# Kernel tuning notes

Hardware: AMD Instinct MI355X
Metric: run time of the kernel (lower is better)

## Reference

```python
import jax, jax.numpy as jnp
import numpy as np

QMAX = 127.0

def setup_inputs() -> dict:
    key = jax.random.key(0)
    kx, kw, ks = jax.random.split(key, 3)
    B, S, D_IN, D_OUT = 4, 2048, 4096, 4096
    x = jax.random.normal(kx, (B, S, D_IN), dtype=jnp.float16)
    # int8 weight buffer, same distribution as torch.randint(-127, 127)
    weight = jax.random.randint(kw, (D_OUT, D_IN), -127, 127, dtype=jnp.int32).astype(jnp.int8)
    # per-output-channel weight scales (fp16 buffer); small positive values
    weight_scales = (jax.random.uniform(ks, (D_OUT,), dtype=jnp.float32) * 0.01 + 1e-4).astype(jnp.float16)
    return {"x": x, "weight": weight, "weight_scales": weight_scales}

def reference(x, weight, weight_scales):
    # x: [B, S, D_in] fp16; weight: [D_out, D_in] int8; weight_scales: [D_out] fp16
    x32 = x.astype(jnp.float32)
    # dynamic per-token absmax quantization: scale = absmax / 127
    absmax = jnp.max(jnp.abs(x32), axis=-1, keepdims=True)      # [B, S, 1]
    x_scales = jnp.maximum(absmax / QMAX, 1e-8)
    q = jnp.round(x32 / x_scales)                                # in [-127, 127]
    q = jnp.clip(q, -QMAX, QMAX).astype(jnp.int8)
    # int8 GEMM accumulated in int32 (cupy.matmul on int32 in the original)
    y = jnp.einsum('bsk,nk->bsn', q.astype(jnp.int32), weight.astype(jnp.int32),
                   preferred_element_type=jnp.int32)             # [B, S, D_out]
    # dequant: per-token activation scale * per-channel weight scale
    y = y.astype(jnp.float32) * x_scales * weight_scales.astype(jnp.float32)[None, None, :]
    return y.astype(jnp.float16)
```

## Files before the change

### kernel.cpp

```cpp
#include <hip/hip_runtime.h>
#include <stdint.h>

typedef int int32x4 __attribute__((ext_vector_type(4)));

constexpr int K_DIM = 4096;
constexpr int N_DIM = 4096;
constexpr float QMAXF = 127.0f;

__global__ __launch_bounds__(256) void quant_rows(const float* __restrict__ x,
                                                  int8_t* __restrict__ q,
                                                  float* __restrict__ scales) {
    const int row = blockIdx.x;
    const int tid = threadIdx.x;
    const size_t base = (size_t)row * K_DIM;

    const float4* xv = reinterpret_cast<const float4*>(x + base);
    float4 v[4];
#pragma unroll
    for (int i = 0; i < 4; ++i) v[i] = xv[tid + 256 * i];

    float m = 0.0f;
#pragma unroll
    for (int i = 0; i < 4; ++i)
        m = fmaxf(m, fmaxf(fmaxf(fabsf(v[i].x), fabsf(v[i].y)),
                           fmaxf(fabsf(v[i].z), fabsf(v[i].w))));
#pragma unroll
    for (int off = 32; off > 0; off >>= 1) m = fmaxf(m, __shfl_xor(m, off));

    __shared__ float wmax[4];
    if ((tid & 63) == 0) wmax[tid >> 6] = m;
    __syncthreads();
    const float am = fmaxf(fmaxf(wmax[0], wmax[1]), fmaxf(wmax[2], wmax[3]));
    const float scale = fmaxf(am * (1.0f / 127.0f), 1e-8f);
    if (tid == 0) scales[row] = scale;
    const float inv = 1.0f / scale;

    int* qw = reinterpret_cast<int*>(q + base);
#pragma unroll
    for (int i = 0; i < 4; ++i) {
        float f0 = fminf(QMAXF, fmaxf(-QMAXF, rintf(v[i].x * inv)));
        float f1 = fminf(QMAXF, fmaxf(-QMAXF, rintf(v[i].y * inv)));
        float f2 = fminf(QMAXF, fmaxf(-QMAXF, rintf(v[i].z * inv)));
        float f3 = fminf(QMAXF, fmaxf(-QMAXF, rintf(v[i].w * inv)));
        int b0 = ((int)f0) & 255, b1 = ((int)f1) & 255;
        int b2 = ((int)f2) & 255, b3 = ((int)f3) & 255;
        qw[tid + 256 * i] = b0 | (b1 << 8) | (b2 << 16) | (b3 << 24);
    }
}

__global__ __launch_bounds__(256) void pack_w(const int* __restrict__ w,
                                              int8_t* __restrict__ w8) {
    const int idx = blockIdx.x * 256 + threadIdx.x;
    const int4 v = reinterpret_cast<const int4*>(w)[idx];
    int packed = (v.x & 255) | ((v.y & 255) << 8) | ((v.z & 255) << 16) | ((v.w & 255) << 24);
    reinterpret_cast<int*>(w8)[idx] = packed;
}

constexpr int BM = 256, BN = 256, BKB = 128;
constexpr int NT = K_DIM / BKB;
constexpr int BSLOT = 32768;

#define GLL(src, dst)                                                          \
    __builtin_amdgcn_global_load_lds(                                          \
        (const __attribute__((address_space(1))) unsigned int*)(src),          \
        (__attribute__((address_space(3))) unsigned int*)(dst), 16, 0, 0)

#define MFMA_I8(a, b, c) __builtin_amdgcn_mfma_i32_16x16x64_i8((a), (b), (c), 0, 0, 0)

__global__ __launch_bounds__(512, 2) void w8a8_flat(
        const int8_t* __restrict__ A, const int8_t* __restrict__ B,
        const float* __restrict__ asc, const float* __restrict__ wsc,
        float* __restrict__ C, int M) {
    extern __shared__ int8_t lds[];

    const int tid  = threadIdx.x;
    const int lane = tid & 63;
    const int wave = tid >> 6;

    const int nwg = gridDim.x;
    const int bid = blockIdx.x;
    const int swz = (bid & 7) * (nwg >> 3) + (bid >> 3);
    const int NB  = N_DIM / BN;
    const int brow = (swz / NB) * BM;
    const int bcol = (swz % NB) * BN;

    const int wm = wave & 3;
    const int wn = wave >> 2;
    const int l15 = lane & 15;
    const int ls  = lane >> 4;

    const int8_t* aglob = A + (size_t)(brow + wm * 64 + l15) * K_DIM + ls * 16;

    const int rowst = tid >> 3;
    const int gsl   = ((tid & 7) ^ (rowst & 7)) * 16;
    const int8_t* gB = B + (size_t)(bcol + rowst) * K_DIM + gsl;
    const size_t chB = (size_t)64 * K_DIM;
    const int segb = wave * 1024;

    const int boff = (wn * 128 + l15) * BKB + ((ls ^ (l15 & 7)) * 16);

    int32x4 acc[4][8];
#pragma unroll
    for (int i = 0; i < 4; ++i)
#pragma unroll
        for (int j = 0; j < 8; ++j) acc[i][j] = (int32x4){0, 0, 0, 0};

    int32x4 avA[8], avB[8];

#pragma unroll
    for (int mi = 0; mi < 4; ++mi) {
        avA[2 * mi]     = *(const int32x4*)(aglob + (size_t)mi * 16 * K_DIM);
        avA[2 * mi + 1] = *(const int32x4*)(aglob + (size_t)mi * 16 * K_DIM + 64);
    }
#pragma unroll
    for (int c = 0; c < 4; ++c) GLL(gB + c * chB, lds + c * 8192 + segb);
#pragma unroll
    for (int c = 0; c < 4; ++c) GLL(gB + 128 + c * chB, lds + BSLOT + c * 8192 + segb);
    asm volatile("s_waitcnt vmcnt(4)" ::: "memory");
    __builtin_amdgcn_s_barrier();

#define TILE_BODY(T, AVC, AVN)                                                 \
    {                                                                          \
        const int8_t* Bb = lds + ((T) % 3) * BSLOT;                            \
        const bool pf1 = ((T) + 1 < NT);                                       \
        const bool pf2 = ((T) + 2 < NT);                                       \
        int32x4 bf[2][2];                                                      \
        bf[0][0] = *(const int32x4*)(Bb + boff);                               \
        bf[0][1] = *(const int32x4*)(Bb + (boff ^ 64));                        \
        _Pragma("unroll")                                                      \
        for (int ni = 0; ni < 8; ++ni) {                                       \
            const int cur = ni & 1, nxt = cur ^ 1;                             \
            if (ni < 4 && pf1) {                                               \
                const int8_t* ap = aglob + ((T) + 1) * 128 +                   \
                                   (size_t)ni * 16 * K_DIM;                    \
                AVN[2 * ni]     = *(const int32x4*)(ap);                       \
                AVN[2 * ni + 1] = *(const int32x4*)(ap + 64);                  \
            }                                                                  \
            if (ni == 4 && pf2) {                                              \
                int8_t* dst = lds + (((T) + 2) % 3) * BSLOT;                   \
                _Pragma("unroll")                                              \
                for (int c = 0; c < 4; ++c)                                    \
                    GLL(gB + ((T) + 2) * 128 + c * chB,                        \
                        dst + c * 8192 + segb);                                \
            }                                                                  \
            if (ni < 7) {                                                      \
                const int o = boff + (ni + 1) * 2048;                          \
                bf[nxt][0] = *(const int32x4*)(Bb + o);                        \
                bf[nxt][1] = *(const int32x4*)(Bb + (o ^ 64));                 \
                asm volatile("s_waitcnt lgkmcnt(2)" ::: "memory");             \
            } else {                                                           \
                asm volatile("s_waitcnt lgkmcnt(0)" ::: "memory");             \
            }                                                                  \
            __builtin_amdgcn_sched_barrier(0);                                 \
            __builtin_amdgcn_s_setprio(1);                                     \
            _Pragma("unroll")                                                  \
            for (int mi = 0; mi < 4; ++mi) {                                   \
                acc[mi][ni] = MFMA_I8(AVC[2 * mi], bf[cur][0], acc[mi][ni]);   \
                acc[mi][ni] = MFMA_I8(AVC[2 * mi + 1], bf[cur][1], acc[mi][ni]); \
            }                                                                  \
            __builtin_amdgcn_s_setprio(0);                                     \
        }                                                                      \
        if ((T) <= NT - 3) asm volatile("s_waitcnt vmcnt(4)" ::: "memory");    \
        else               asm volatile("s_waitcnt vmcnt(0)" ::: "memory");    \
        __builtin_amdgcn_sched_barrier(0);                                     \
        __builtin_amdgcn_s_barrier();                                          \
    }

    for (int t = 0; t < NT; t += 2) {
        TILE_BODY(t,     avA, avB);
        TILE_BODY(t + 1, avB, avA);
    }

    const int c0  = lane & 15;
    const int rr0 = (lane >> 4) * 4;
#pragma unroll
    for (int ni = 0; ni < 8; ++ni) {
        const int col = bcol + wn * 128 + ni * 16 + c0;
        const float ws = wsc[col];
#pragma unroll
        for (int mi = 0; mi < 4; ++mi) {
            const int rowb = brow + wm * 64 + mi * 16 + rr0;
#pragma unroll
            for (int r = 0; r < 4; ++r) {
                const int row = rowb + r;
                float o = (float)acc[mi][ni][r] * asc[row] * ws;
                o = (float)(_Float16)o;
                C[(size_t)row * N_DIM + col] = o;
            }
        }
    }
}

extern "C" void kernel_launch(void* const* d_in, const int* in_sizes, int n_in,
                              void* d_out, int out_size, void* d_ws, size_t ws_size,
                              hipStream_t stream) {
    const float* x   = (const float*)d_in[0];
    const int*   w   = (const int*)d_in[1];
    const float* wsc = (const float*)d_in[2];
    float* out = (float*)d_out;

    const int K = K_DIM;
    const int M = in_sizes[0] / K;
    const int N = N_DIM;

    int8_t* q   = (int8_t*)d_ws;
    int8_t* w8  = (int8_t*)d_ws + (size_t)M * K;
    float*  asc = (float*)((char*)d_ws + (size_t)M * K + (size_t)N * K);

    quant_rows<<<M, 256, 0, stream>>>(x, q, asc);
    pack_w<<<(N * (K / 4)) / 256, 256, 0, stream>>>(w, w8);
    const int grid = (M / BM) * (N / BN);
    w8a8_flat<<<grid, 512, 98304, stream>>>(q, w8, asc, wsc, out, M);
}
```

Before: 222.5 us.

## Quantize activations into MFMA-fragment-ordered layout for coalesced A loads

The quantization kernel now handles 16 rows per block, staging the int8 results in shared memory and writing them in a tiled order. In that order each wave's 64 lanes read one contiguous 1 KB chunk per MFMA A fragment, replacing strided per-row loads in the GEMM. The GEMM's A addressing is rewritten to match, and the end-of-tile vmcnt wait is relaxed to allow more outstanding loads. The quant kernel now reads x twice and uses 64 KB of LDS per block, and the relaxed vmcnt condition adds ordering risk.

```diff
diff --git a/kernel.cpp b/kernel.cpp
--- a/kernel.cpp
+++ b/kernel.cpp
@@ -7,44 +7,57 @@
 constexpr int N_DIM = 4096;
 constexpr float QMAXF = 127.0f;
 
-__global__ __launch_bounds__(256) void quant_rows(const float* __restrict__ x,
-                                                  int8_t* __restrict__ q,
-                                                  float* __restrict__ scales) {
-    const int row = blockIdx.x;
+__global__ __launch_bounds__(256) void quant_t(const float* __restrict__ x,
+                                               int8_t* __restrict__ qt,
+                                               float* __restrict__ scales) {
+    __shared__ int8_t lq[16][4112];
+    const int b = blockIdx.x;
     const int tid = threadIdx.x;
-    const size_t base = (size_t)row * K_DIM;
-
-    const float4* xv = reinterpret_cast<const float4*>(x + base);
-    float4 v[4];
-#pragma unroll
-    for (int i = 0; i < 4; ++i) v[i] = xv[tid + 256 * i];
+    const int row16 = tid >> 4;
+    const int j = tid & 15;
+    const size_t rbase = ((size_t)b * 16 + row16) * K_DIM;
+    const float4* xr = reinterpret_cast<const float4*>(x + rbase);
 
     float m = 0.0f;
-#pragma unroll
-    for (int i = 0; i < 4; ++i)
-        m = fmaxf(m, fmaxf(fmaxf(fabsf(v[i].x), fabsf(v[i].y)),
-                           fmaxf(fabsf(v[i].z), fabsf(v[i].w))));
-#pragma unroll
-    for (int off = 32; off > 0; off >>= 1) m = fmaxf(m, __shfl_xor(m, off));
-
-    __shared__ float wmax[4];
-    if ((tid & 63) == 0) wmax[tid >> 6] = m;
+#pragma unroll 4
+    for (int i = 0; i < 16; ++i) {
+        const int c = j + 16 * i;
+#pragma unroll
+        for (int s = 0; s < 4; ++s) {
+            float4 v = xr[c * 4 + s];
+            m = fmaxf(m, fmaxf(fmaxf(fabsf(v.x), fabsf(v.y)),
+                               fmaxf(fabsf(v.z), fabsf(v.w))));
+        }
+    }
+#pragma unroll
+    for (int off = 8; off > 0; off >>= 1) m = fmaxf(m, __shfl_xor(m, off));
+    const float scale = fmaxf(m * (1.0f / 127.0f), 1e-8f);
+    if (j == 0) scales[b * 16 + row16] = scale;
+    const float inv = 1.0f / scale;
+
+#pragma unroll 4
+    for (int i = 0; i < 16; ++i) {
+        const int c = j + 16 * i;
+        int w[4];
+#pragma unroll
+        for (int s = 0; s < 4; ++s) {
+            float4 v = xr[c * 4 + s];
+            int b0 = ((int)fminf(QMAXF, fmaxf(-QMAXF, rintf(v.x * inv)))) & 255;
+            int b1 = ((int)fminf(QMAXF, fmaxf(-QMAXF, rintf(v.y * inv)))) & 255;
+            int b2 = ((int)fminf(QMAXF, fmaxf(-QMAXF, rintf(v.z * inv)))) & 255;
+            int b3 = ((int)fminf(QMAXF, fmaxf(-QMAXF, rintf(v.w * inv)))) & 255;
+            w[s] = b0 | (b1 << 8) | (b2 << 16) | (b3 << 24);
+        }
+        *reinterpret_cast<int32x4*>(&lq[row16][c * 16]) = (int32x4){w[0], w[1], w[2], w[3]};
+    }
     __syncthreads();
-    const float am = fmaxf(fmaxf(wmax[0], wmax[1]), fmaxf(wmax[2], wmax[3]));
-    const float scale = fmaxf(am * (1.0f / 127.0f), 1e-8f);
-    if (tid == 0) scales[row] = scale;
-    const float inv = 1.0f / scale;
-
-    int* qw = reinterpret_cast<int*>(q + base);
-#pragma unroll
-    for (int i = 0; i < 4; ++i) {
-        float f0 = fminf(QMAXF, fmaxf(-QMAXF, rintf(v[i].x * inv)));
-        float f1 = fminf(QMAXF, fmaxf(-QMAXF, rintf(v[i].y * inv)));
-        float f2 = fminf(QMAXF, fmaxf(-QMAXF, rintf(v[i].z * inv)));
-        float f3 = fminf(QMAXF, fmaxf(-QMAXF, rintf(v[i].w * inv)));
-        int b0 = ((int)f0) & 255, b1 = ((int)f1) & 255;
-        int b2 = ((int)f2) & 255, b3 = ((int)f3) & 255;
-        qw[tid + 256 * i] = b0 | (b1 << 8) | (b2 << 16) | (b3 << 24);
+
+    int8_t* outp = qt + (size_t)b * 65536;
+#pragma unroll
+    for (int i = 0; i < 16; ++i) {
+        const int u = tid + 256 * i;
+        int32x4 v = *reinterpret_cast<const int32x4*>(&lq[u & 15][(u >> 4) * 16]);
+        *reinterpret_cast<int32x4*>(outp + (size_t)u * 16) = v;
     }
 }
 
@@ -68,7 +81,7 @@
 #define MFMA_I8(a, b, c) __builtin_amdgcn_mfma_i32_16x16x64_i8((a), (b), (c), 0, 0, 0)
 
 __global__ __launch_bounds__(512, 2) void w8a8_flat(
-        const int8_t* __restrict__ A, const int8_t* __restrict__ B,
+        const int8_t* __restrict__ QT, const int8_t* __restrict__ B,
         const float* __restrict__ asc, const float* __restrict__ wsc,
         float* __restrict__ C, int M) {
     extern __shared__ int8_t lds[];
@@ -89,7 +102,7 @@
     const int l15 = lane & 15;
     const int ls  = lane >> 4;
 
-    const int8_t* aglob = A + (size_t)(brow + wm * 64 + l15) * K_DIM + ls * 16;
+    const int8_t* qa = QT + (size_t)(brow >> 4) * 65536 + lane * 16;
 
     const int rowst = tid >> 3;
     const int gsl   = ((tid & 7) ^ (rowst & 7)) * 16;
@@ -109,8 +122,9 @@
 
 #pragma unroll
     for (int mi = 0; mi < 4; ++mi) {
-        avA[2 * mi]     = *(const int32x4*)(aglob + (size_t)mi * 16 * K_DIM);
-        avA[2 * mi + 1] = *(const int32x4*)(aglob + (size_t)mi * 16 * K_DIM + 64);
+        const int8_t* ap = qa + (((wm * 4 + mi) * 64) << 10);
+        avA[2 * mi]     = *(const int32x4*)(ap);
+        avA[2 * mi + 1] = *(const int32x4*)(ap + 1024);
     }
 #pragma unroll
     for (int c = 0; c < 4; ++c) GLL(gB + c * chB, lds + c * 8192 + segb);
@@ -131,10 +145,10 @@
         for (int ni = 0; ni < 8; ++ni) {                                       \
             const int cur = ni & 1, nxt = cur ^ 1;                             \
             if (ni < 4 && pf1) {                                               \
-                const int8_t* ap = aglob + ((T) + 1) * 128 +                   \
-                                   (size_t)ni * 16 * K_DIM;                    \
+                const int8_t* ap = qa +                                        \
+                    ((((wm * 4 + ni) * 64) + ((T) + 1) * 2) << 10);            \
                 AVN[2 * ni]     = *(const int32x4*)(ap);                       \
-                AVN[2 * ni + 1] = *(const int32x4*)(ap + 64);                  \
+                AVN[2 * ni + 1] = *(const int32x4*)(ap + 1024);                \
             }                                                                  \
             if (ni == 4 && pf2) {                                              \
                 int8_t* dst = lds + (((T) + 2) % 3) * BSLOT;                   \
@@ -160,8 +174,8 @@
             }                                                                  \
             __builtin_amdgcn_s_setprio(0);                                     \
         }                                                                      \
-        if ((T) <= NT - 3) asm volatile("s_waitcnt vmcnt(4)" ::: "memory");    \
-        else               asm volatile("s_waitcnt vmcnt(0)" ::: "memory");    \
+        if ((T) < NT - 1) asm volatile("s_waitcnt vmcnt(8)" ::: "memory");     \
+        else              asm volatile("s_waitcnt vmcnt(0)" ::: "memory");     \
         __builtin_amdgcn_sched_barrier(0);                                     \
         __builtin_amdgcn_s_barrier();                                          \
     }
@@ -203,12 +217,12 @@
     const int M = in_sizes[0] / K;
     const int N = N_DIM;
 
-    int8_t* q   = (int8_t*)d_ws;
+    int8_t* qt  = (int8_t*)d_ws;
     int8_t* w8  = (int8_t*)d_ws + (size_t)M * K;
     float*  asc = (float*)((char*)d_ws + (size_t)M * K + (size_t)N * K);
 
-    quant_rows<<<M, 256, 0, stream>>>(x, q, asc);
+    quant_t<<<M / 16, 256, 0, stream>>>(x, qt, asc);
     pack_w<<<(N * (K / 4)) / 256, 256, 0, stream>>>(w, w8);
     const int grid = (M / BM) * (N / BN);
-    w8a8_flat<<<grid, 512, 98304, stream>>>(q, w8, asc, wsc, out, M);
-}
+    w8a8_flat<<<grid, 512, 98304, stream>>>(qt, w8, asc, wsc, out, M);
+}
```

Result: faster. 206.7 us (-7.1%).
